# Kernel optimization log

Hardware: AMD Instinct MI355X
Metric: run time of the kernel (lower is better)

The kernel has to match this reference:

```python
import jax, jax.numpy as jnp
import numpy as np

EMB = 64
RNN = 128


def _lstm_scan(x_tbe, Wx, Wh, b, reverse=False):
    # x_tbe: [T, B, E] -> hidden states [T, B, H]; Keras gate order i, f, g(c), o
    B = x_tbe.shape[1]
    H = Wh.shape[0]

    def step(carry, xt):
        h, c = carry
        z = xt @ Wx + h @ Wh + b  # [B, 4H]
        i, f, g, o = jnp.split(z, 4, axis=-1)
        c = jax.nn.sigmoid(f) * c + jax.nn.sigmoid(i) * jnp.tanh(g)
        h = jax.nn.sigmoid(o) * jnp.tanh(c)
        return (h, c), h

    init = (jnp.zeros((B, H), x_tbe.dtype), jnp.zeros((B, H), x_tbe.dtype))
    _, hs = jax.lax.scan(step, init, x_tbe, reverse=reverse)
    return hs  # outputs aligned with input time indices


def _crf_log_likelihood(logits, labels, lengths, T):
    # logits: [B, L, K], labels: [B, L] int, lengths: [B] int, T: [K, K]
    B, L, K = logits.shape
    pos = jnp.arange(L)[None, :] < lengths[:, None]  # [B, L] bool
    posf = pos.astype(logits.dtype)
    # unary score: sum of logits at gold labels over valid positions
    unary = jnp.sum(jnp.take_along_axis(logits, labels[..., None], axis=2)[..., 0] * posf, axis=1)
    # binary score: transition t -> t+1 counted iff position t+1 is valid
    binary = jnp.sum(T[labels[:, :-1], labels[:, 1:]] * posf[:, 1:], axis=1)
    # forward algorithm (log partition), masked recurrence over time
    def step(alphas, inp):
        logit_t, m_t = inp  # [B, K], [B] bool
        new = jax.nn.logsumexp(alphas[:, :, None] + T[None], axis=1) + logit_t
        return jnp.where(m_t[:, None], new, alphas), None

    xs = (jnp.transpose(logits[:, 1:], (1, 0, 2)), jnp.transpose(pos[:, 1:]))
    alphas, _ = jax.lax.scan(step, logits[:, 0], xs)
    log_norm = jax.nn.logsumexp(alphas, axis=1)
    return unary + binary - log_norm


def setup_inputs() -> dict:
    key = jax.random.key(0)
    ks = jax.random.split(key, 12)
    B, L, V, K = 512, 256, 30001, 18
    inputs = jax.random.randint(ks[0], (B, L), 0, V)
    labels = jax.random.randint(ks[1], (B, L), 0, K)
    E = jax.random.normal(ks[2], (V, EMB), dtype=jnp.float32) * 0.1
    Wx_f = jax.random.normal(ks[3], (EMB, 4 * RNN), dtype=jnp.float32) * 0.05
    Wh_f = jax.random.normal(ks[4], (RNN, 4 * RNN), dtype=jnp.float32) * 0.05
    b_f = jnp.zeros((4 * RNN,), jnp.float32)
    Wx_b = jax.random.normal(ks[5], (EMB, 4 * RNN), dtype=jnp.float32) * 0.05
    Wh_b = jax.random.normal(ks[6], (RNN, 4 * RNN), dtype=jnp.float32) * 0.05
    b_b = jnp.zeros((4 * RNN,), jnp.float32)
    Wd = jax.random.normal(ks[7], (2 * RNN, K), dtype=jnp.float32) * 0.05
    bd = jnp.zeros((K,), jnp.float32)
    T = jax.random.uniform(ks[8], (K, K), dtype=jnp.float32)
    return dict(inputs=inputs, labels=labels, E=E, Wx_f=Wx_f, Wh_f=Wh_f, b_f=b_f,
                Wx_b=Wx_b, Wh_b=Wh_b, b_b=b_b, Wd=Wd, bd=bd, T=T)


def reference(inputs, labels, E, Wx_f, Wh_f, b_f, Wx_b, Wh_b, b_b, Wd, bd, T):
    emb = E[inputs]  # [B, L, EMB]
    x = jnp.transpose(emb, (1, 0, 2))  # [L, B, EMB]
    h_fwd = _lstm_scan(x, Wx_f, Wh_f, b_f, reverse=False)
    h_bwd = _lstm_scan(x, Wx_b, Wh_b, b_b, reverse=True)
    h = jnp.concatenate([h_fwd, h_bwd], axis=-1)  # [L, B, 2*RNN]
    logits = jnp.transpose(h, (1, 0, 2)) @ Wd + bd  # [B, L, K]
    lengths = jnp.sum((labels != 0).astype(jnp.int32), axis=1)
    log_likelihood = _crf_log_likelihood(logits, labels, lengths, T)
    return log_likelihood, T
```

## Files before the change

### kernel.cpp

```cpp
#include <hip/hip_runtime.h>
#include <stdint.h>

#define BATCH 512
#define SEQ   256
#define EMBD  64
#define HID   128
#define GATES 512
#define NST   18
#define LROW  (BATCH * NST)

typedef short  bf16x8 __attribute__((ext_vector_type(8)));
typedef float  f32x4  __attribute__((ext_vector_type(4)));

__device__ __forceinline__ short f2bf(float f) {
  unsigned u = __float_as_uint(f);
  u = (u + 0x7FFFu + ((u >> 16) & 1u)) >> 16;
  return (short)u;
}
__device__ __forceinline__ float rcpf(float x) { return __builtin_amdgcn_rcpf(x); }

__device__ __forceinline__ void lds_barrier() {
  __builtin_amdgcn_sched_barrier(0);
  asm volatile("s_waitcnt lgkmcnt(0)");
  __builtin_amdgcn_s_barrier();
  __builtin_amdgcn_sched_barrier(0);
}

__global__ void k_embed(const int* __restrict__ inputs, const float* __restrict__ E,
                        short* __restrict__ emb) {
  int tid = blockIdx.x * 256 + threadIdx.x;
  int e4 = (tid & 15) << 2;
  int b  = (tid >> 4) & (BATCH - 1);
  int t  = tid >> 13;
  int vid = inputs[b * SEQ + t];
  float4 v = *reinterpret_cast<const float4*>(E + (size_t)vid * EMBD + e4);
  short4 o;
  o.x = f2bf(v.x); o.y = f2bf(v.y); o.z = f2bf(v.z); o.w = f2bf(v.w);
  *reinterpret_cast<short4*>(emb + (size_t)(t * BATCH + b) * EMBD + e4) = o;
}

__global__ void __launch_bounds__(512)
__attribute__((amdgpu_waves_per_eu(2, 2)))
k_lstm(const short* __restrict__ emb,
       const float* __restrict__ Wx_f, const float* __restrict__ Wh_f, const float* __restrict__ b_f,
       const float* __restrict__ Wx_b, const float* __restrict__ Wh_b, const float* __restrict__ b_b,
       const float* __restrict__ Wd,
       float* __restrict__ logits_f, float* __restrict__ logits_b) {
  const int blk  = blockIdx.x;
  const int dir  = blk & 1;
  const int b0   = (blk >> 1) * 4;
  const int tid  = threadIdx.x;
  const int w    = tid >> 6;
  const int lane = tid & 63;
  const int quad = lane >> 4;
  const int mrow = lane & 15;
  const int arow = mrow >> 2;
  const int hcol = w * 16 + mrow;
  const int erow = b0 + arow;

  const float* WX = dir ? Wx_b : Wx_f;
  const float* WH = dir ? Wh_b : Wh_f;
  const float* BV = dir ? b_b  : b_f;
  float* LOG = dir ? logits_b : logits_f;

  bf16x8 wxf[4][2], whf[4][4], wdf[4];
  float bias[4];
#pragma unroll
  for (int q = 0; q < 4; ++q) {
    int col = q * HID + hcol;
    bias[q] = BV[col];
#pragma unroll
    for (int kt = 0; kt < 2; ++kt) {
      bf16x8 f;
#pragma unroll
      for (int j = 0; j < 8; ++j) {
        int k = kt * 32 + quad * 8 + j;
        f[j] = f2bf(WX[k * GATES + col]);
      }
      wxf[q][kt] = f;
    }
#pragma unroll
    for (int kt = 0; kt < 4; ++kt) {
      bf16x8 f;
#pragma unroll
      for (int j = 0; j < 8; ++j) {
        int k = kt * 32 + quad * 8 + j;
        f[j] = f2bf(WH[k * GATES + col]);
      }
      whf[q][kt] = f;
    }
  }
  const int  lcol = w * 16 + mrow;
  const bool lw   = (w < 2);
  const bool lval = lw && (lcol < NST);
#pragma unroll
  for (int kt = 0; kt < 4; ++kt) {
    bf16x8 f;
#pragma unroll
    for (int j = 0; j < 8; ++j) {
      int k = kt * 32 + quad * 8 + j;
      f[j] = lval ? f2bf(Wd[(dir * HID + k) * NST + lcol]) : (short)0;
    }
    wdf[kt] = f;
  }

  __shared__ __align__(16) short hbuf[2][4 * 128];
  if (tid < 256) {
    int* p = reinterpret_cast<int*>(hbuf);
    p[tid] = 0;
    p[tid + 256] = 0;
  }
  __syncthreads();

  float c = 0.f;
  float la[8];
#pragma unroll
  for (int i = 0; i < 8; ++i) la[i] = 0.f;

  const int t0 = dir ? (SEQ - 1) : 0;
  const short* efp0 = emb + ((size_t)(t0 * BATCH + erow) * EMBD + quad * 8);
  bf16x8 xa0 = *reinterpret_cast<const bf16x8*>(efp0);
  bf16x8 xa1 = *reinterpret_cast<const bf16x8*>(efp0 + 32);

  for (int so = 0; so < SEQ; so += 8) {
#pragma unroll
    for (int si = 0; si < 8; ++si) {
      const int s = so + si;
      const int p = s & 1;
      const int sn = (s + 1 < SEQ) ? s + 1 : s;
      const int tn = dir ? (SEQ - 1 - sn) : sn;
      const short* efp = emb + ((size_t)(tn * BATCH + erow) * EMBD + quad * 8);
      bf16x8 xb0 = *reinterpret_cast<const bf16x8*>(efp);
      bf16x8 xb1 = *reinterpret_cast<const bf16x8*>(efp + 32);

      bf16x8 hfr[4];
      const char* hb = reinterpret_cast<const char*>(hbuf[p ^ 1]);
#pragma unroll
      for (int kt = 0; kt < 4; ++kt) {
        unsigned off = (unsigned)(arow * 256 + kt * 64 + quad * 16) ^ ((unsigned)arow << 5);
        hfr[kt] = *reinterpret_cast<const bf16x8*>(hb + off);
      }

      f32x4 za[4], zb[4];
#pragma unroll
      for (int q = 0; q < 4; ++q) {
        f32x4 a = {bias[q], bias[q], bias[q], bias[q]};
        a = __builtin_amdgcn_mfma_f32_16x16x32_bf16(xa0, wxf[q][0], a, 0, 0, 0);
        f32x4 b2 = {0.f, 0.f, 0.f, 0.f};
        b2 = __builtin_amdgcn_mfma_f32_16x16x32_bf16(xa1, wxf[q][1], b2, 0, 0, 0);
        a  = __builtin_amdgcn_mfma_f32_16x16x32_bf16(hfr[0], whf[q][0], a, 0, 0, 0);
        b2 = __builtin_amdgcn_mfma_f32_16x16x32_bf16(hfr[2], whf[q][2], b2, 0, 0, 0);
        a  = __builtin_amdgcn_mfma_f32_16x16x32_bf16(hfr[1], whf[q][1], a, 0, 0, 0);
        b2 = __builtin_amdgcn_mfma_f32_16x16x32_bf16(hfr[3], whf[q][3], b2, 0, 0, 0);
        za[q] = a; zb[q] = b2;
      }

      float zi = za[0][0] + zb[0][0];
      float zf = za[1][0] + zb[1][0];
      float zg = za[2][0] + zb[2][0];
      float zo = za[3][0] + zb[3][0];
      float ei  = __expf(-zi);
      float e2g = __expf(-2.f * zg);
      float ef  = __expf(-zf);
      float fg  = rcpf(1.f + ef);
      float it  = (1.f - e2g) * rcpf((1.f + ei) * (1.f + e2g));
      float cn  = fg * c + it;
      c = cn;
      float eo  = __expf(-zo);
      float e2c = __expf(-2.f * cn);
      short hv = f2bf((1.f - e2c) * rcpf((1.f + eo) * (1.f + e2c)));

      {
        char* wb = reinterpret_cast<char*>(hbuf[p]);
        unsigned off = (unsigned)(quad * 256 + hcol * 2) ^ ((unsigned)quad << 5);
        *reinterpret_cast<short*>(wb + off) = hv;
      }

      if (lw && (so + si) > 0) {
        f32x4 l = {0.f, 0.f, 0.f, 0.f};
#pragma unroll
        for (int kt = 0; kt < 4; ++kt)
          l = __builtin_amdgcn_mfma_f32_16x16x32_bf16(hfr[kt], wdf[kt], l, 0, 0, 0);
        la[si] = l[0];
      }

      lds_barrier();
      xa0 = xb0; xa1 = xb1;
    }

    if (lval) {
#pragma unroll
      for (int si = 0; si < 8; ++si) {
        if (so == 0 && si == 0) continue;
        int pos = dir ? (SEQ - so - si) : (so + si - 1);
        LOG[(size_t)pos * LROW + (size_t)(b0 + quad) * NST + lcol] = la[si];
      }
    }
  }

  if (lw) {
    const char* hb = reinterpret_cast<const char*>(hbuf[(SEQ - 1) & 1]);
    bf16x8 hfr[4];
#pragma unroll
    for (int kt = 0; kt < 4; ++kt) {
      unsigned off = (unsigned)(arow * 256 + kt * 64 + quad * 16) ^ ((unsigned)arow << 5);
      hfr[kt] = *reinterpret_cast<const bf16x8*>(hb + off);
    }
    f32x4 l = {0.f, 0.f, 0.f, 0.f};
#pragma unroll
    for (int kt = 0; kt < 4; ++kt)
      l = __builtin_amdgcn_mfma_f32_16x16x32_bf16(hfr[kt], wdf[kt], l, 0, 0, 0);
    int tp = dir ? 0 : (SEQ - 1);
    if (lval)
      LOG[(size_t)tp * LROW + (size_t)(b0 + quad) * NST + lcol] = l[0];
  }
}

__global__ void k_crf(const float* __restrict__ lf, const float* __restrict__ lb,
                      const float* __restrict__ bd, const float* __restrict__ Tm,
                      const int* __restrict__ labels, float* __restrict__ out) {
  const int wv   = threadIdx.x >> 6;
  const int lane = threadIdx.x & 63;
  const int b    = blockIdx.x * 2 + wv;
  __shared__ unsigned char lab[2][SEQ];

  int4 lv = *reinterpret_cast<const int4*>(labels + (size_t)b * SEQ + lane * 4);
  uchar4 lc;
  lc.x = (unsigned char)lv.x; lc.y = (unsigned char)lv.y;
  lc.z = (unsigned char)lv.z; lc.w = (unsigned char)lv.w;
  *reinterpret_cast<uchar4*>(&lab[wv][lane * 4]) = lc;
  int cnt = (lv.x != 0) + (lv.y != 0) + (lv.z != 0) + (lv.w != 0);
#pragma unroll
  for (int d = 32; d; d >>= 1) cnt += __shfl_xor(cnt, d);
  const int len = cnt;

  float ub = 0.f;
#pragma unroll
  for (int ii = 0; ii < 4; ++ii) {
    int p = ii * 64 + lane;
    int lp = lab[wv][p];
    if (p < len) {
      size_t o = (size_t)p * LROW + (size_t)b * NST + lp;
      ub += lf[o] + lb[o] + bd[lp];
    }
    if (p < SEQ - 1 && (p + 1) < len)
      ub += Tm[lp * NST + lab[wv][p + 1]];
  }
#pragma unroll
  for (int d = 32; d; d >>= 1) ub += __shfl_xor(ub, d);

  const int h9 = lane >> 5;
  const int j  = lane & 31;
  const int jj = (j < NST) ? j : 0;
  float Tcol[9];
#pragma unroll
  for (int i2 = 0; i2 < 9; ++i2) Tcol[i2] = Tm[(9 * h9 + i2) * NST + jj];
  const float bdj = bd[jj];
  const size_t rowoff = (size_t)b * NST + jj;

  float alpha = lf[rowoff] + lb[rowoff] + bdj;

  float pfa[8], pfb[8];
#pragma unroll
  for (int u = 0; u < 8; ++u) {
    size_t o = (size_t)(1 + u) * LROW + rowoff;
    pfa[u] = lf[o]; pfb[u] = lb[o];
  }

  for (int tb = 1; tb < len; tb += 8) {
#pragma unroll
    for (int u = 0; u < 8; ++u) {
      int t = tb + u;
      if (t < len) {
        float lg = pfa[u] + pfb[u] + bdj;
        float tt[9];
#pragma unroll
        for (int i2 = 0; i2 < 9; ++i2)
          tt[i2] = __shfl(alpha, 9 * h9 + i2) + Tcol[i2];
        float ma = fmaxf(fmaxf(tt[0], tt[1]), fmaxf(tt[2], tt[3]));
        float mb = fmaxf(fmaxf(tt[4], tt[5]), fmaxf(tt[6], tt[7]));
        float m9 = fmaxf(fmaxf(ma, mb), tt[8]);
        float s0 = __expf(tt[0] - m9) + __expf(tt[1] - m9);
        float s1 = __expf(tt[2] - m9) + __expf(tt[3] - m9);
        float s2 = __expf(tt[4] - m9) + __expf(tt[5] - m9);
        float s3 = __expf(tt[6] - m9) + __expf(tt[7] - m9);
        float s9 = ((s0 + s1) + (s2 + s3)) + __expf(tt[8] - m9);
        float mo = __shfl_xor(m9, 32);
        float so = __shfl_xor(s9, 32);
        float m  = fmaxf(m9, mo);
        float s  = s9 * __expf(m9 - m) + so * __expf(mo - m);
        alpha = m + __logf(s) + lg;
      }
      int tn = t + 8; if (tn > SEQ - 1) tn = SEQ - 1;
      size_t o = (size_t)tn * LROW + rowoff;
      pfa[u] = lf[o]; pfb[u] = lb[o];
    }
  }

  float v = (lane < NST) ? alpha : -1e30f;
  float mm = v;
#pragma unroll
  for (int d = 32; d; d >>= 1) mm = fmaxf(mm, __shfl_xor(mm, d));
  float e = (lane < NST) ? __expf(alpha - mm) : 0.f;
#pragma unroll
  for (int d = 32; d; d >>= 1) e += __shfl_xor(e, d);
  if (lane == 0) out[b] = ub - (mm + __logf(e));
}

__global__ void k_tcopy(const float* __restrict__ Tm, float* __restrict__ out) {
  int i = blockIdx.x * 256 + threadIdx.x;
  if (i < NST * NST) out[BATCH + i] = Tm[i];
}

extern "C" void kernel_launch(void* const* d_in, const int* in_sizes, int n_in,
                              void* d_out, int out_size, void* d_ws, size_t ws_size,
                              hipStream_t stream) {
  const int*   inputs = (const int*)d_in[0];
  const int*   labels = (const int*)d_in[1];
  const float* E      = (const float*)d_in[2];
  const float* Wx_f   = (const float*)d_in[3];
  const float* Wh_f   = (const float*)d_in[4];
  const float* b_f    = (const float*)d_in[5];
  const float* Wx_b   = (const float*)d_in[6];
  const float* Wh_b   = (const float*)d_in[7];
  const float* b_b    = (const float*)d_in[8];
  const float* Wd     = (const float*)d_in[9];
  const float* bd     = (const float*)d_in[10];
  const float* Tm     = (const float*)d_in[11];
  float* out = (float*)d_out;

  char* ws = (char*)d_ws;
  short* emb      = (short*)ws;
  float* logits_f = (float*)(ws + (size_t)16777216);
  float* logits_b = (float*)(ws + (size_t)16777216 + 9437184);

  k_embed<<<8192, 256, 0, stream>>>(inputs, E, emb);
  k_lstm<<<256, 512, 0, stream>>>(emb, Wx_f, Wh_f, b_f, Wx_b, Wh_b, b_b, Wd,
                                  logits_f, logits_b);
  k_crf<<<256, 128, 0, stream>>>(logits_f, logits_b, bd, Tm, labels, out);
  k_tcopy<<<2, 256, 0, stream>>>(Tm, out);
}
```

Measured before the change: 329.6 us.

## Split CRF partition into forward and backward half-recurrences meeting in the middle

The CRF log-partition recurrence is now split across two waves per sequence: one runs the forward alpha recursion up to the midpoint and the other runs a backward beta recursion from the end down to it. The two are combined with a logsumexp after a block barrier, roughly halving the serial dependency chain per sequence. The LSTM kernel also keeps its MFMA accumulators persistent across steps and only resets the lane element that is read, to reduce register moves. The CRF block size doubles, and the mathematically equivalent reordering may change rounding slightly.

```diff
diff --git a/kernel.cpp b/kernel.cpp
--- a/kernel.cpp
+++ b/kernel.cpp
@@ -117,6 +117,14 @@
 #pragma unroll
   for (int i = 0; i < 8; ++i) la[i] = 0.f;
 
+  f32x4 za[4], zb[4], lacc;
+#pragma unroll
+  for (int q = 0; q < 4; ++q) {
+    za[q][0] = 0.f; za[q][1] = 0.f; za[q][2] = 0.f; za[q][3] = 0.f;
+    zb[q] = za[q];
+  }
+  lacc[0] = 0.f; lacc[1] = 0.f; lacc[2] = 0.f; lacc[3] = 0.f;
+
   const int t0 = dir ? (SEQ - 1) : 0;
   const short* efp0 = emb + ((size_t)(t0 * BATCH + erow) * EMBD + quad * 8);
   bf16x8 xa0 = *reinterpret_cast<const bf16x8*>(efp0);
@@ -141,18 +149,16 @@
         hfr[kt] = *reinterpret_cast<const bf16x8*>(hb + off);
       }
 
-      f32x4 za[4], zb[4];
 #pragma unroll
       for (int q = 0; q < 4; ++q) {
-        f32x4 a = {bias[q], bias[q], bias[q], bias[q]};
-        a = __builtin_amdgcn_mfma_f32_16x16x32_bf16(xa0, wxf[q][0], a, 0, 0, 0);
-        f32x4 b2 = {0.f, 0.f, 0.f, 0.f};
-        b2 = __builtin_amdgcn_mfma_f32_16x16x32_bf16(xa1, wxf[q][1], b2, 0, 0, 0);
-        a  = __builtin_amdgcn_mfma_f32_16x16x32_bf16(hfr[0], whf[q][0], a, 0, 0, 0);
-        b2 = __builtin_amdgcn_mfma_f32_16x16x32_bf16(hfr[2], whf[q][2], b2, 0, 0, 0);
-        a  = __builtin_amdgcn_mfma_f32_16x16x32_bf16(hfr[1], whf[q][1], a, 0, 0, 0);
-        b2 = __builtin_amdgcn_mfma_f32_16x16x32_bf16(hfr[3], whf[q][3], b2, 0, 0, 0);
-        za[q] = a; zb[q] = b2;
+        za[q][0] = bias[q];
+        zb[q][0] = 0.f;
+        za[q] = __builtin_amdgcn_mfma_f32_16x16x32_bf16(xa0, wxf[q][0], za[q], 0, 0, 0);
+        zb[q] = __builtin_amdgcn_mfma_f32_16x16x32_bf16(xa1, wxf[q][1], zb[q], 0, 0, 0);
+        za[q] = __builtin_amdgcn_mfma_f32_16x16x32_bf16(hfr[0], whf[q][0], za[q], 0, 0, 0);
+        zb[q] = __builtin_amdgcn_mfma_f32_16x16x32_bf16(hfr[2], whf[q][2], zb[q], 0, 0, 0);
+        za[q] = __builtin_amdgcn_mfma_f32_16x16x32_bf16(hfr[1], whf[q][1], za[q], 0, 0, 0);
+        zb[q] = __builtin_amdgcn_mfma_f32_16x16x32_bf16(hfr[3], whf[q][3], zb[q], 0, 0, 0);
       }
 
       float zi = za[0][0] + zb[0][0];
@@ -177,11 +183,11 @@
       }
 
       if (lw && (so + si) > 0) {
-        f32x4 l = {0.f, 0.f, 0.f, 0.f};
+        lacc[0] = 0.f;
 #pragma unroll
         for (int kt = 0; kt < 4; ++kt)
-          l = __builtin_amdgcn_mfma_f32_16x16x32_bf16(hfr[kt], wdf[kt], l, 0, 0, 0);
-        la[si] = l[0];
+          lacc = __builtin_amdgcn_mfma_f32_16x16x32_bf16(hfr[kt], wdf[kt], lacc, 0, 0, 0);
+        la[si] = lacc[0];
       }
 
       lds_barrier();
@@ -206,105 +212,158 @@
       unsigned off = (unsigned)(arow * 256 + kt * 64 + quad * 16) ^ ((unsigned)arow << 5);
       hfr[kt] = *reinterpret_cast<const bf16x8*>(hb + off);
     }
-    f32x4 l = {0.f, 0.f, 0.f, 0.f};
+    lacc[0] = 0.f;
 #pragma unroll
     for (int kt = 0; kt < 4; ++kt)
-      l = __builtin_amdgcn_mfma_f32_16x16x32_bf16(hfr[kt], wdf[kt], l, 0, 0, 0);
+      lacc = __builtin_amdgcn_mfma_f32_16x16x32_bf16(hfr[kt], wdf[kt], lacc, 0, 0, 0);
     int tp = dir ? 0 : (SEQ - 1);
     if (lval)
-      LOG[(size_t)tp * LROW + (size_t)(b0 + quad) * NST + lcol] = l[0];
+      LOG[(size_t)tp * LROW + (size_t)(b0 + quad) * NST + lcol] = lacc[0];
   }
 }
 
 __global__ void k_crf(const float* __restrict__ lf, const float* __restrict__ lb,
                       const float* __restrict__ bd, const float* __restrict__ Tm,
                       const int* __restrict__ labels, float* __restrict__ out) {
-  const int wv   = threadIdx.x >> 6;
-  const int lane = threadIdx.x & 63;
-  const int b    = blockIdx.x * 2 + wv;
+  const int wv    = threadIdx.x >> 6;
+  const int rsel  = wv >> 1;
+  const int isBwd = wv & 1;
+  const int lane  = threadIdx.x & 63;
+  const int b     = blockIdx.x * 2 + rsel;
   __shared__ unsigned char lab[2][SEQ];
+  __shared__ float redA[2][NST], redB[2][NST], ubv[2];
 
   int4 lv = *reinterpret_cast<const int4*>(labels + (size_t)b * SEQ + lane * 4);
-  uchar4 lc;
-  lc.x = (unsigned char)lv.x; lc.y = (unsigned char)lv.y;
-  lc.z = (unsigned char)lv.z; lc.w = (unsigned char)lv.w;
-  *reinterpret_cast<uchar4*>(&lab[wv][lane * 4]) = lc;
   int cnt = (lv.x != 0) + (lv.y != 0) + (lv.z != 0) + (lv.w != 0);
 #pragma unroll
   for (int d = 32; d; d >>= 1) cnt += __shfl_xor(cnt, d);
   const int len = cnt;
-
-  float ub = 0.f;
-#pragma unroll
-  for (int ii = 0; ii < 4; ++ii) {
-    int p = ii * 64 + lane;
-    int lp = lab[wv][p];
-    if (p < len) {
-      size_t o = (size_t)p * LROW + (size_t)b * NST + lp;
-      ub += lf[o] + lb[o] + bd[lp];
-    }
-    if (p < SEQ - 1 && (p + 1) < len)
-      ub += Tm[lp * NST + lab[wv][p + 1]];
-  }
-#pragma unroll
-  for (int d = 32; d; d >>= 1) ub += __shfl_xor(ub, d);
+  const int tm  = (len - 1) >> 1;
 
   const int h9 = lane >> 5;
   const int j  = lane & 31;
   const int jj = (j < NST) ? j : 0;
-  float Tcol[9];
-#pragma unroll
-  for (int i2 = 0; i2 < 9; ++i2) Tcol[i2] = Tm[(9 * h9 + i2) * NST + jj];
   const float bdj = bd[jj];
   const size_t rowoff = (size_t)b * NST + jj;
 
-  float alpha = lf[rowoff] + lb[rowoff] + bdj;
-
-  float pfa[8], pfb[8];
-#pragma unroll
-  for (int u = 0; u < 8; ++u) {
-    size_t o = (size_t)(1 + u) * LROW + rowoff;
-    pfa[u] = lf[o]; pfb[u] = lb[o];
-  }
-
-  for (int tb = 1; tb < len; tb += 8) {
+  if (!isBwd) {
+    uchar4 lc;
+    lc.x = (unsigned char)lv.x; lc.y = (unsigned char)lv.y;
+    lc.z = (unsigned char)lv.z; lc.w = (unsigned char)lv.w;
+    *reinterpret_cast<uchar4*>(&lab[rsel][lane * 4]) = lc;
+    float ub = 0.f;
+#pragma unroll
+    for (int ii = 0; ii < 4; ++ii) {
+      int p = ii * 64 + lane;
+      int lp = lab[rsel][p];
+      if (p < len) {
+        size_t o = (size_t)p * LROW + (size_t)b * NST + lp;
+        ub += lf[o] + lb[o] + bd[lp];
+      }
+      if (p < SEQ - 1 && (p + 1) < len)
+        ub += Tm[lp * NST + lab[rsel][p + 1]];
+    }
+#pragma unroll
+    for (int d = 32; d; d >>= 1) ub += __shfl_xor(ub, d);
+    if (lane == 0) ubv[rsel] = ub;
+
+    float Tcol[9];
+#pragma unroll
+    for (int i2 = 0; i2 < 9; ++i2) Tcol[i2] = Tm[(9 * h9 + i2) * NST + jj];
+    float alpha = lf[rowoff] + lb[rowoff] + bdj;
+    float pfa[8], pfb[8];
 #pragma unroll
     for (int u = 0; u < 8; ++u) {
-      int t = tb + u;
-      if (t < len) {
-        float lg = pfa[u] + pfb[u] + bdj;
-        float tt[9];
-#pragma unroll
-        for (int i2 = 0; i2 < 9; ++i2)
-          tt[i2] = __shfl(alpha, 9 * h9 + i2) + Tcol[i2];
-        float ma = fmaxf(fmaxf(tt[0], tt[1]), fmaxf(tt[2], tt[3]));
-        float mb = fmaxf(fmaxf(tt[4], tt[5]), fmaxf(tt[6], tt[7]));
-        float m9 = fmaxf(fmaxf(ma, mb), tt[8]);
-        float s0 = __expf(tt[0] - m9) + __expf(tt[1] - m9);
-        float s1 = __expf(tt[2] - m9) + __expf(tt[3] - m9);
-        float s2 = __expf(tt[4] - m9) + __expf(tt[5] - m9);
-        float s3 = __expf(tt[6] - m9) + __expf(tt[7] - m9);
-        float s9 = ((s0 + s1) + (s2 + s3)) + __expf(tt[8] - m9);
-        float mo = __shfl_xor(m9, 32);
-        float so = __shfl_xor(s9, 32);
-        float m  = fmaxf(m9, mo);
-        float s  = s9 * __expf(m9 - m) + so * __expf(mo - m);
-        alpha = m + __logf(s) + lg;
-      }
-      int tn = t + 8; if (tn > SEQ - 1) tn = SEQ - 1;
-      size_t o = (size_t)tn * LROW + rowoff;
+      int ti = 1 + u; if (ti > SEQ - 1) ti = SEQ - 1;
+      size_t o = (size_t)ti * LROW + rowoff;
       pfa[u] = lf[o]; pfb[u] = lb[o];
     }
-  }
-
-  float v = (lane < NST) ? alpha : -1e30f;
-  float mm = v;
-#pragma unroll
-  for (int d = 32; d; d >>= 1) mm = fmaxf(mm, __shfl_xor(mm, d));
-  float e = (lane < NST) ? __expf(alpha - mm) : 0.f;
-#pragma unroll
-  for (int d = 32; d; d >>= 1) e += __shfl_xor(e, d);
-  if (lane == 0) out[b] = ub - (mm + __logf(e));
+    for (int tb = 1; tb <= tm; tb += 8) {
+#pragma unroll
+      for (int u = 0; u < 8; ++u) {
+        int t = tb + u;
+        if (t <= tm) {
+          float lg = pfa[u] + pfb[u] + bdj;
+          float tt[9];
+#pragma unroll
+          for (int i2 = 0; i2 < 9; ++i2)
+            tt[i2] = __shfl(alpha, 9 * h9 + i2) + Tcol[i2];
+          float ma = fmaxf(fmaxf(tt[0], tt[1]), fmaxf(tt[2], tt[3]));
+          float mb = fmaxf(fmaxf(tt[4], tt[5]), fmaxf(tt[6], tt[7]));
+          float m9 = fmaxf(fmaxf(ma, mb), tt[8]);
+          float s0 = __expf(tt[0] - m9) + __expf(tt[1] - m9);
+          float s1 = __expf(tt[2] - m9) + __expf(tt[3] - m9);
+          float s2 = __expf(tt[4] - m9) + __expf(tt[5] - m9);
+          float s3 = __expf(tt[6] - m9) + __expf(tt[7] - m9);
+          float s9 = ((s0 + s1) + (s2 + s3)) + __expf(tt[8] - m9);
+          float mo = __shfl_xor(m9, 32);
+          float so = __shfl_xor(s9, 32);
+          float m  = fmaxf(m9, mo);
+          float s  = s9 * __expf(m9 - m) + so * __expf(mo - m);
+          alpha = m + __logf(s) + lg;
+        }
+        int ti = t + 8; if (ti > SEQ - 1) ti = SEQ - 1;
+        size_t o = (size_t)ti * LROW + rowoff;
+        pfa[u] = lf[o]; pfb[u] = lb[o];
+      }
+    }
+    if (lane < NST) redA[rsel][lane] = alpha;
+  } else {
+    float Trow[9];
+#pragma unroll
+    for (int i2 = 0; i2 < 9; ++i2) Trow[i2] = Tm[jj * NST + 9 * h9 + i2];
+    float beta = 0.f;
+    float pfa[8], pfb[8];
+#pragma unroll
+    for (int u = 0; u < 8; ++u) {
+      int ti = len - 1 - u; if (ti < 0) ti = 0;
+      size_t o = (size_t)ti * LROW + rowoff;
+      pfa[u] = lf[o]; pfb[u] = lb[o];
+    }
+    for (int tb = len - 2; tb >= tm; tb -= 8) {
+#pragma unroll
+      for (int u = 0; u < 8; ++u) {
+        int t = tb - u;
+        if (t >= tm) {
+          float gj = beta + (pfa[u] + pfb[u] + bdj);
+          float tt[9];
+#pragma unroll
+          for (int i2 = 0; i2 < 9; ++i2)
+            tt[i2] = __shfl(gj, 9 * h9 + i2) + Trow[i2];
+          float ma = fmaxf(fmaxf(tt[0], tt[1]), fmaxf(tt[2], tt[3]));
+          float mb = fmaxf(fmaxf(tt[4], tt[5]), fmaxf(tt[6], tt[7]));
+          float m9 = fmaxf(fmaxf(ma, mb), tt[8]);
+          float s0 = __expf(tt[0] - m9) + __expf(tt[1] - m9);
+          float s1 = __expf(tt[2] - m9) + __expf(tt[3] - m9);
+          float s2 = __expf(tt[4] - m9) + __expf(tt[5] - m9);
+          float s3 = __expf(tt[6] - m9) + __expf(tt[7] - m9);
+          float s9 = ((s0 + s1) + (s2 + s3)) + __expf(tt[8] - m9);
+          float mo = __shfl_xor(m9, 32);
+          float so = __shfl_xor(s9, 32);
+          float m  = fmaxf(m9, mo);
+          float s  = s9 * __expf(m9 - m) + so * __expf(mo - m);
+          beta = m + __logf(s);
+        }
+        int ti = t + 1 - 8; if (ti < 0) ti = 0;
+        size_t o = (size_t)ti * LROW + rowoff;
+        pfa[u] = lf[o]; pfb[u] = lb[o];
+      }
+    }
+    if (lane < NST) redB[rsel][lane] = beta;
+  }
+
+  __syncthreads();
+
+  if (wv < 2) {
+    float v = (lane < NST) ? redA[wv][lane] + redB[wv][lane] : -1e30f;
+    float mm = v;
+#pragma unroll
+    for (int d = 32; d; d >>= 1) mm = fmaxf(mm, __shfl_xor(mm, d));
+    float e = (lane < NST) ? __expf(v - mm) : 0.f;
+#pragma unroll
+    for (int d = 32; d; d >>= 1) e += __shfl_xor(e, d);
+    if (lane == 0) out[blockIdx.x * 2 + wv] = ubv[wv] - (mm + __logf(e));
+  }
 }
 
 __global__ void k_tcopy(const float* __restrict__ Tm, float* __restrict__ out) {
@@ -337,6 +396,6 @@
   k_embed<<<8192, 256, 0, stream>>>(inputs, E, emb);
   k_lstm<<<256, 512, 0, stream>>>(emb, Wx_f, Wh_f, b_f, Wx_b, Wh_b, b_b, Wd,
                                   logits_f, logits_b);
-  k_crf<<<256, 128, 0, stream>>>(logits_f, logits_b, bd, Tm, labels, out);
+  k_crf<<<256, 256, 0, stream>>>(logits_f, logits_b, bd, Tm, labels, out);
   k_tcopy<<<2, 256, 0, stream>>>(Tm, out);
 }
```

Result: faster. 296.0 us (-10.2%).
